# Kernel tuning notes

Measured on AMD Instinct MI355X. Metric: run time of the kernel, lower is better.

Reference implementation:

```python
import jax, jax.numpy as jnp
import numpy as np

# DLMLayer (breadth=2) forward, soft/dense path.
# Group arities: 0 (nullary [B,C0]), 1 (unary [B,n,C1]), 2 (binary [B,n,n,C2]).
# Per group i: concat [Expand(inputs[i-1]), inputs[i], Reduce(inputs[i+1])],
# then Permutation(i) (concat over i! axis permutations), then logic MLP
# (Linear -> sigmoid) over the channel dim. exclude_self masks the diagonal
# in the binary->unary reduction (max filled with 0, min filled with 1,
# valid for probabilistic truth values in [0,1]).

def setup_inputs() -> dict:
    key = jax.random.key(0)
    ks = jax.random.split(key, 9)
    B, n, C = 16, 128, 64
    x0 = jax.random.uniform(ks[0], (B, 8), dtype=jnp.float32)
    x1 = jax.random.uniform(ks[1], (B, n, C), dtype=jnp.float32)
    x2 = jax.random.uniform(ks[2], (B, n, n, C), dtype=jnp.float32)
    # current_dim per group: i=0: 8 + 2*64 = 136 ; i=1: 8 + 64 + 2*64 = 200 (1!=1)
    # i=2: (64 + 64) * 2! = 256
    W0 = jax.random.normal(ks[3], (136, C), dtype=jnp.float32) * 0.1
    W1 = jax.random.normal(ks[4], (200, C), dtype=jnp.float32) * 0.1
    W2 = jax.random.normal(ks[5], (256, C), dtype=jnp.float32) * 0.1
    b0 = jnp.zeros((C,), jnp.float32)
    b1 = jnp.zeros((C,), jnp.float32)
    b2 = jnp.zeros((C,), jnp.float32)
    return {"x0": x0, "x1": x1, "x2": x2, "W0": W0, "b0": b0,
            "W1": W1, "b1": b1, "W2": W2, "b2": b2}


def reference(x0, x1, x2, W0, b0, W1, b1, W2, b2):
    B, n, C = x1.shape
    # ---- group 0 (nullary): input x0 + reduce(x1) over the object axis ----
    r1 = jnp.concatenate([x1.max(axis=1), x1.min(axis=1)], axis=-1)  # [B, 2C]
    f0 = jnp.concatenate([x0, r1], axis=-1)                          # [B, 136]
    out0 = jax.nn.sigmoid(f0 @ W0 + b0)                              # [B, C]
    # ---- group 1 (unary): expand x0, input x1, reduce x2 (exclude self) ----
    e0 = jnp.broadcast_to(x0[:, None, :], (B, n, x0.shape[-1]))      # [B, n, 8]
    diag = jnp.eye(n, dtype=bool)[None, :, :, None]                  # [1, n, n, 1]
    rmax = jnp.where(diag, 0.0, x2).max(axis=2)                      # [B, n, C]
    rmin = jnp.where(diag, 1.0, x2).min(axis=2)                      # [B, n, C]
    f1 = jnp.concatenate([e0, x1, rmax, rmin], axis=-1)              # [B, n, 200]
    out1 = jax.nn.sigmoid(f1 @ W1 + b1)                              # [B, n, C]
    # ---- group 2 (binary): expand x1, input x2, permute axes (1,2) ----
    e1 = jnp.broadcast_to(x1[:, :, None, :], (B, n, n, C))           # [B, n, n, C]
    g = jnp.concatenate([e1, x2], axis=-1)                           # [B, n, n, 2C]
    f2 = jnp.concatenate([g, jnp.swapaxes(g, 1, 2)], axis=-1)        # [B, n, n, 4C]
    out2 = jax.nn.sigmoid(f2 @ W2 + b2)                              # [B, n, n, C]
    return (out0, out1, out2)
```

## Files before the change

kernel.cpp:

```cpp
#include <hip/hip_runtime.h>
#include <hip/hip_bf16.h>
#include <cstdint>


#define NDIM 128
#define CDIM 64

typedef float f32x4 __attribute__((ext_vector_type(4)));
typedef short s16x8 __attribute__((ext_vector_type(8)));

__device__ __forceinline__ unsigned short f2bf(float f) {
    union { float f; unsigned int u; } v; v.f = f;
    unsigned int u = v.u;
    return (unsigned short)((u + 0x7FFFu + ((u >> 16) & 1u)) >> 16);
}
__device__ __forceinline__ float sigmoidf_(float x) {
    return 1.0f / (1.0f + __expf(-x));
}

__global__ __launch_bounds__(256) void k_prep(const float* __restrict__ x0,
        const float* __restrict__ x1, const float* __restrict__ W0,
        const float* __restrict__ b0, const float* __restrict__ W2,
        const float* __restrict__ b2, float* __restrict__ PA,
        float* __restrict__ PB, unsigned short* __restrict__ WT,
        float* __restrict__ out0) {
    int bb = blockIdx.x;
    int t = threadIdx.x;
    if (bb < 512) {
        int u = t >> 6, c = t & 63;
        int blk = bb * 4 + u;
        __shared__ float xv[4][64];
        xv[u][c] = x1[blk * 64 + c];
        float accA = b2[c];
        float accB = 0.f;
#pragma unroll 8
        for (int k = 0; k < 64; ++k) {
            float xk = xv[u][k];
            accA += xk * W2[k * 64 + c];
            accB += xk * W2[(128 + k) * 64 + c];
        }
        PA[blk * 64 + c] = accA;
        PB[blk * 64 + c] = accB;
    } else if (bb < 544) {
        int idx = (bb - 512) * 256 + t;
        int n = idx >> 7, k = idx & 127;
        int row = (k < 64) ? (64 + k) : (128 + k);
        WT[idx] = f2bf(W2[row * 64 + n]);
    } else {
        int b = bb - 544;
        int lane = t & 63, w = t >> 6;
        int q = lane & 15;
        int jq = lane >> 4;
        __shared__ float pw[4][64], pn[4][64], f0[136], spart[4][64];
        f32x4 mx = {-1e30f, -1e30f, -1e30f, -1e30f};
        f32x4 mn = {1e30f, 1e30f, 1e30f, 1e30f};
#pragma unroll
        for (int p = 0; p < 8; ++p) {
            int j = (w * 4 + jq) + 16 * p;
            float4 v = *reinterpret_cast<const float4*>(
                x1 + ((size_t)(b * 128 + j)) * 64 + q * 4);
            mx.x = fmaxf(mx.x, v.x); mx.y = fmaxf(mx.y, v.y);
            mx.z = fmaxf(mx.z, v.z); mx.w = fmaxf(mx.w, v.w);
            mn.x = fminf(mn.x, v.x); mn.y = fminf(mn.y, v.y);
            mn.z = fminf(mn.z, v.z); mn.w = fminf(mn.w, v.w);
        }
#pragma unroll
        for (int d = 16; d <= 32; d <<= 1) {
            mx.x = fmaxf(mx.x, __shfl_xor(mx.x, d)); mx.y = fmaxf(mx.y, __shfl_xor(mx.y, d));
            mx.z = fmaxf(mx.z, __shfl_xor(mx.z, d)); mx.w = fmaxf(mx.w, __shfl_xor(mx.w, d));
            mn.x = fminf(mn.x, __shfl_xor(mn.x, d)); mn.y = fminf(mn.y, __shfl_xor(mn.y, d));
            mn.z = fminf(mn.z, __shfl_xor(mn.z, d)); mn.w = fminf(mn.w, __shfl_xor(mn.w, d));
        }
        if (lane < 16) {
            *reinterpret_cast<f32x4*>(&pw[w][lane * 4]) = mx;
            *reinterpret_cast<f32x4*>(&pn[w][lane * 4]) = mn;
        }
        __syncthreads();
        if (t < 64) {
            int c = t;
            float M = fmaxf(fmaxf(pw[0][c], pw[1][c]), fmaxf(pw[2][c], pw[3][c]));
            float m = fminf(fminf(pn[0][c], pn[1][c]), fminf(pn[2][c], pn[3][c]));
            f0[8 + c] = M; f0[72 + c] = m;
            if (c < 8) f0[c] = x0[b * 8 + c];
        }
        __syncthreads();
        {
            int g = t >> 6, c = t & 63;
            float acc = 0.f;
#pragma unroll
            for (int k = g * 34; k < g * 34 + 34; ++k) acc += f0[k] * W0[k * 64 + c];
            spart[g][c] = acc;
        }
        __syncthreads();
        if (t < 64) {
            int c = t;
            out0[b * 64 + c] = sigmoidf_(
                spart[0][c] + spart[1][c] + spart[2][c] + spart[3][c] + b0[c]);
        }
    }
}

__global__ __launch_bounds__(128) void k_main(const float* __restrict__ x2,
        const unsigned short* __restrict__ WT,
        const float* __restrict__ PA, const float* __restrict__ PB,
        float* __restrict__ pmax_ws, float* __restrict__ pmin_ws,
        float* __restrict__ out2) {
    int bid = blockIdx.x;
    int blk = bid >> 1, half = bid & 1;
    int b = blk >> 7, i = blk & 127;
    int j0 = half << 6;
    int t = threadIdx.x;
    int lane = t & 63, w = t >> 6;
    int jq = lane >> 4;
    int cc = (lane & 15) * 4;

    __shared__ __align__(16) unsigned short Ald[64 * 128];

    const float* xaSrc = x2 + (size_t)blk * (NDIM * CDIM);

    float4 va[8];
#pragma unroll
    for (int p = 0; p < 8; ++p) {
        int jl = 32 * w + p * 4 + jq;
        va[p] = *reinterpret_cast<const float4*>(xaSrc + (j0 + jl) * 64 + cc);
    }
    f32x4 mx = {0.f, 0.f, 0.f, 0.f}, mn = {1.f, 1.f, 1.f, 1.f};
#pragma unroll
    for (int p = 0; p < 8; ++p) {
        int jl = 32 * w + p * 4 + jq;
        bool ok = (j0 + jl != i);
        mx.x = fmaxf(mx.x, ok ? va[p].x : 0.0f); mx.y = fmaxf(mx.y, ok ? va[p].y : 0.0f);
        mx.z = fmaxf(mx.z, ok ? va[p].z : 0.0f); mx.w = fmaxf(mx.w, ok ? va[p].w : 0.0f);
        mn.x = fminf(mn.x, ok ? va[p].x : 1.0f); mn.y = fminf(mn.y, ok ? va[p].y : 1.0f);
        mn.z = fminf(mn.z, ok ? va[p].z : 1.0f); mn.w = fminf(mn.w, ok ? va[p].w : 1.0f);
        ushort4 u;
        u.x = f2bf(va[p].x); u.y = f2bf(va[p].y); u.z = f2bf(va[p].z); u.w = f2bf(va[p].w);
        *reinterpret_cast<ushort4*>(&Ald[jl * 128 + (cc ^ ((jl & 7) << 3))]) = u;
    }
#pragma unroll
    for (int d = 16; d <= 32; d <<= 1) {
        mx.x = fmaxf(mx.x, __shfl_xor(mx.x, d)); mx.y = fmaxf(mx.y, __shfl_xor(mx.y, d));
        mx.z = fmaxf(mx.z, __shfl_xor(mx.z, d)); mx.w = fmaxf(mx.w, __shfl_xor(mx.w, d));
        mn.x = fminf(mn.x, __shfl_xor(mn.x, d)); mn.y = fminf(mn.y, __shfl_xor(mn.y, d));
        mn.z = fminf(mn.z, __shfl_xor(mn.z, d)); mn.w = fminf(mn.w, __shfl_xor(mn.w, d));
    }
    if (lane < 16) {
        int slot = blk * 4 + half * 2 + w;
        *reinterpret_cast<f32x4*>(&pmax_ws[slot * 64 + cc]) = mx;
        *reinterpret_cast<f32x4*>(&pmin_ws[slot * 64 + cc]) = mn;
    }

#pragma unroll
    for (int p = 0; p < 8; ++p) {
        int jl = 32 * w + p * 4 + jq;
        float4 v = *reinterpret_cast<const float4*>(
            x2 + ((size_t)((b * 128 + j0 + jl) * 128 + i)) * 64 + cc);
        ushort4 u;
        u.x = f2bf(v.x); u.y = f2bf(v.y); u.z = f2bf(v.z); u.w = f2bf(v.w);
        *reinterpret_cast<ushort4*>(&Ald[jl * 128 + ((64 + cc) ^ ((jl & 7) << 3))]) = u;
    }

    s16x8 bfrag[4][4];
#pragma unroll
    for (int ks = 0; ks < 4; ++ks)
#pragma unroll
        for (int nt = 0; nt < 4; ++nt) {
            int n = nt * 16 + (lane & 15);
            int k0 = ks * 32 + jq * 8;
            bfrag[ks][nt] = *reinterpret_cast<const s16x8*>(WT + n * 128 + k0);
        }

    f32x4 acc[2][4];
#pragma unroll
    for (int m = 0; m < 2; ++m)
#pragma unroll
        for (int nt = 0; nt < 4; ++nt) acc[m][nt] = (f32x4){0.f, 0.f, 0.f, 0.f};

    asm volatile("s_waitcnt lgkmcnt(0)" ::: "memory");
    __builtin_amdgcn_sched_barrier(0);

#pragma unroll
    for (int ks = 0; ks < 4; ++ks) {
#pragma unroll
        for (int m = 0; m < 2; ++m) {
            int rowl = 32 * w + m * 16 + (lane & 15);
            int u8 = (ks * 4 + jq) * 8;
            s16x8 afrag = *reinterpret_cast<const s16x8*>(
                &Ald[rowl * 128 + (u8 ^ ((rowl & 7) << 3))]);
#pragma unroll
            for (int nt = 0; nt < 4; ++nt)
                acc[m][nt] = __builtin_amdgcn_mfma_f32_16x16x32_bf16(
                    afrag, bfrag[ks][nt], acc[m][nt], 0, 0, 0);
        }
    }

    const float* PAi = PA + blk * 64;
    const float* PBb = PB + b * 128 * 64;
    float* outBase = out2 + (size_t)blk * (NDIM * CDIM);
#pragma unroll
    for (int m = 0; m < 2; ++m) {
        int jt = j0 + 32 * w + m * 16 + jq * 4;
#pragma unroll
        for (int nt = 0; nt < 4; ++nt) {
            int cp = nt * 16 + (lane & 15);
            float pav = PAi[cp];
#pragma unroll
            for (int r = 0; r < 4; ++r) {
                int j = jt + r;
                outBase[j * 64 + cp] = sigmoidf_(acc[m][nt][r] + pav + PBb[j * 64 + cp]);
            }
        }
    }
}

__global__ __launch_bounds__(256) void k_out1_tail(const float* __restrict__ x0,
        const float* __restrict__ x1, const float* __restrict__ W1,
        const float* __restrict__ b1, const float* __restrict__ pmax_ws,
        const float* __restrict__ pmin_ws, float* __restrict__ out1) {
    int blk = blockIdx.x;
    int t = threadIdx.x;
    int c = t & 63, g = t >> 6;
    __shared__ float sf[200], spart[4][64];
    if (t < 64) {
        float M = 0.f, m = 1.f;
#pragma unroll
        for (int s = 0; s < 4; ++s) {
            M = fmaxf(M, pmax_ws[(blk * 4 + s) * 64 + c]);
            m = fminf(m, pmin_ws[(blk * 4 + s) * 64 + c]);
        }
        sf[72 + c] = M; sf[136 + c] = m;
        sf[8 + c] = x1[blk * 64 + c];
        if (c < 8) sf[c] = x0[(blk >> 7) * 8 + c];
    }
    __syncthreads();
    {
        float a = 0.f;
#pragma unroll 10
        for (int k = g * 50; k < g * 50 + 50; ++k) a += sf[k] * W1[k * 64 + c];
        spart[g][c] = a;
    }
    __syncthreads();
    if (t < 64) {
        out1[blk * 64 + c] = sigmoidf_(
            spart[0][c] + spart[1][c] + spart[2][c] + spart[3][c] + b1[c]);
    }
}

extern "C" void kernel_launch(void* const* d_in, const int* in_sizes, int n_in,
                              void* d_out, int out_size, void* d_ws, size_t ws_size,
                              hipStream_t stream) {
    const float* x0 = (const float*)d_in[0];
    const float* x1 = (const float*)d_in[1];
    const float* x2 = (const float*)d_in[2];
    const float* W0 = (const float*)d_in[3];
    const float* b0 = (const float*)d_in[4];
    const float* W1 = (const float*)d_in[5];
    const float* b1 = (const float*)d_in[6];
    const float* W2 = (const float*)d_in[7];
    const float* b2 = (const float*)d_in[8];

    float* out0 = (float*)d_out;
    float* out1 = out0 + 16 * 64;
    float* out2 = out1 + 16 * 128 * 64;

    float* PA = (float*)d_ws;
    float* PB = PA + 16 * 128 * 64;
    unsigned short* WT = (unsigned short*)(PB + 16 * 128 * 64);
    float* pmax_ws = (float*)(WT + 64 * 128);
    float* pmin_ws = pmax_ws + 2048 * 4 * 64;

    k_prep<<<560, 256, 0, stream>>>(x0, x1, W0, b0, W2, b2, PA, PB, WT, out0);
    k_main<<<4096, 128, 0, stream>>>(x2, WT, PA, PB, pmax_ws, pmin_ws, out2);
    k_out1_tail<<<2048, 256, 0, stream>>>(x0, x1, W1, b1, pmax_ws, pmin_ws, out1);
}
```

Measured before the change: 52.82 us.

## Split binary-group GEMM into halves to overlap transposed loads with MFMA

The strided transposed x2 loads are now issued early into registers, and the first half of the K dimension (the direct x2 half) is computed with MFMA while those loads are in flight. After that the second half is converted and written to LDS and its MFMAs run. Bf16 conversion also switches from manual bit rounding to the packed v_cvt_pk_bf16_f32 instruction. This adds register pressure (32 more VGPRs for vb plus split B fragments), which could reduce occupancy.

Result: no change. 53.30 us (+0.9%).

```diff
diff --git a/kernel.cpp b/kernel.cpp
--- a/kernel.cpp
+++ b/kernel.cpp
@@ -16,6 +16,12 @@
 }
 __device__ __forceinline__ float sigmoidf_(float x) {
     return 1.0f / (1.0f + __expf(-x));
+}
+__device__ __forceinline__ uint2 pk4(float4 v) {
+    unsigned lo, hi;
+    asm("v_cvt_pk_bf16_f32 %0, %1, %2" : "=v"(lo) : "v"(v.x), "v"(v.y));
+    asm("v_cvt_pk_bf16_f32 %0, %1, %2" : "=v"(hi) : "v"(v.z), "v"(v.w));
+    uint2 r; r.x = lo; r.y = hi; return r;
 }
 
 __global__ __launch_bounds__(256) void k_prep(const float* __restrict__ x0,
@@ -133,10 +139,18 @@
         mx.z = fmaxf(mx.z, ok ? va[p].z : 0.0f); mx.w = fmaxf(mx.w, ok ? va[p].w : 0.0f);
         mn.x = fminf(mn.x, ok ? va[p].x : 1.0f); mn.y = fminf(mn.y, ok ? va[p].y : 1.0f);
         mn.z = fminf(mn.z, ok ? va[p].z : 1.0f); mn.w = fminf(mn.w, ok ? va[p].w : 1.0f);
-        ushort4 u;
-        u.x = f2bf(va[p].x); u.y = f2bf(va[p].y); u.z = f2bf(va[p].z); u.w = f2bf(va[p].w);
-        *reinterpret_cast<ushort4*>(&Ald[jl * 128 + (cc ^ ((jl & 7) << 3))]) = u;
-    }
+        uint2 u = pk4(va[p]);
+        *reinterpret_cast<uint2*>(&Ald[jl * 128 + (cc ^ ((jl & 7) << 3))]) = u;
+    }
+
+    float4 vb[8];
+#pragma unroll
+    for (int p = 0; p < 8; ++p) {
+        int jl = 32 * w + p * 4 + jq;
+        vb[p] = *reinterpret_cast<const float4*>(
+            x2 + ((size_t)((b * 128 + j0 + jl) * 128 + i)) * 64 + cc);
+    }
+
 #pragma unroll
     for (int d = 16; d <= 32; d <<= 1) {
         mx.x = fmaxf(mx.x, __shfl_xor(mx.x, d)); mx.y = fmaxf(mx.y, __shfl_xor(mx.y, d));
@@ -150,24 +164,13 @@
         *reinterpret_cast<f32x4*>(&pmin_ws[slot * 64 + cc]) = mn;
     }
 
-#pragma unroll
-    for (int p = 0; p < 8; ++p) {
-        int jl = 32 * w + p * 4 + jq;
-        float4 v = *reinterpret_cast<const float4*>(
-            x2 + ((size_t)((b * 128 + j0 + jl) * 128 + i)) * 64 + cc);
-        ushort4 u;
-        u.x = f2bf(v.x); u.y = f2bf(v.y); u.z = f2bf(v.z); u.w = f2bf(v.w);
-        *reinterpret_cast<ushort4*>(&Ald[jl * 128 + ((64 + cc) ^ ((jl & 7) << 3))]) = u;
-    }
-
-    s16x8 bfrag[4][4];
-#pragma unroll
-    for (int ks = 0; ks < 4; ++ks)
+    s16x8 bf01[2][4];
+#pragma unroll
+    for (int ks = 0; ks < 2; ++ks)
 #pragma unroll
         for (int nt = 0; nt < 4; ++nt) {
             int n = nt * 16 + (lane & 15);
-            int k0 = ks * 32 + jq * 8;
-            bfrag[ks][nt] = *reinterpret_cast<const s16x8*>(WT + n * 128 + k0);
+            bf01[ks][nt] = *reinterpret_cast<const s16x8*>(WT + n * 128 + ks * 32 + jq * 8);
         }
 
     f32x4 acc[2][4];
@@ -180,7 +183,7 @@
     __builtin_amdgcn_sched_barrier(0);
 
 #pragma unroll
-    for (int ks = 0; ks < 4; ++ks) {
+    for (int ks = 0; ks < 2; ++ks) {
 #pragma unroll
         for (int m = 0; m < 2; ++m) {
             int rowl = 32 * w + m * 16 + (lane & 15);
@@ -190,7 +193,41 @@
 #pragma unroll
             for (int nt = 0; nt < 4; ++nt)
                 acc[m][nt] = __builtin_amdgcn_mfma_f32_16x16x32_bf16(
-                    afrag, bfrag[ks][nt], acc[m][nt], 0, 0, 0);
+                    afrag, bf01[ks][nt], acc[m][nt], 0, 0, 0);
+        }
+    }
+
+#pragma unroll
+    for (int p = 0; p < 8; ++p) {
+        int jl = 32 * w + p * 4 + jq;
+        uint2 u = pk4(vb[p]);
+        *reinterpret_cast<uint2*>(&Ald[jl * 128 + ((64 + cc) ^ ((jl & 7) << 3))]) = u;
+    }
+    s16x8 bf23[2][4];
+#pragma unroll
+    for (int ks = 0; ks < 2; ++ks)
+#pragma unroll
+        for (int nt = 0; nt < 4; ++nt) {
+            int n = nt * 16 + (lane & 15);
+            bf23[ks][nt] = *reinterpret_cast<const s16x8*>(
+                WT + n * 128 + (2 + ks) * 32 + jq * 8);
+        }
+
+    asm volatile("s_waitcnt lgkmcnt(0)" ::: "memory");
+    __builtin_amdgcn_sched_barrier(0);
+
+#pragma unroll
+    for (int ks = 0; ks < 2; ++ks) {
+#pragma unroll
+        for (int m = 0; m < 2; ++m) {
+            int rowl = 32 * w + m * 16 + (lane & 15);
+            int u8 = ((2 + ks) * 4 + jq) * 8;
+            s16x8 afrag = *reinterpret_cast<const s16x8*>(
+                &Ald[rowl * 128 + (u8 ^ ((rowl & 7) << 3))]);
+#pragma unroll
+            for (int nt = 0; nt < 4; ++nt)
+                acc[m][nt] = __builtin_amdgcn_mfma_f32_16x16x32_bf16(
+                    afrag, bf23[ks][nt], acc[m][nt], 0, 0, 0);
         }
     }
 
```

## Build MFMA fragments directly from registers, drop LDS staging, swizzle block order

Applied to the files above, without the earlier changes.

The main kernel no longer stages bf16-converted x2 rows through shared memory. Each lane now loads exactly the fp32 elements it needs for the MFMA operand and packs them with v_cvt_pk_bf16_f32. The GEMM is transposed so that weights are the A operand and data rows the B operand, which lets the epilogue write out2 with vectorized float4 stores. The masked max/min reduction is reworked to use a shuffle pattern that fits the new lane layout, and block IDs are remapped to change L2 locality. This removes LDS traffic and the waitcnt barrier, but the per-lane loads are less coalesced (eight floats per lane per row) and the scalar pmax/pmin stores go through fewer lanes.

Result: slower. 67.46 us (+27.7%).

```diff
diff --git a/kernel.cpp b/kernel.cpp
--- a/kernel.cpp
+++ b/kernel.cpp
@@ -16,6 +16,18 @@
 }
 __device__ __forceinline__ float sigmoidf_(float x) {
     return 1.0f / (1.0f + __expf(-x));
+}
+__device__ __forceinline__ uint2 pk4(float4 v) {
+    unsigned lo, hi;
+    asm("v_cvt_pk_bf16_f32 %0, %1, %2" : "=v"(lo) : "v"(v.x), "v"(v.y));
+    asm("v_cvt_pk_bf16_f32 %0, %1, %2" : "=v"(hi) : "v"(v.z), "v"(v.w));
+    uint2 r; r.x = lo; r.y = hi; return r;
+}
+__device__ __forceinline__ s16x8 mkfrag(float4 a, float4 b) {
+    uint2 p = pk4(a), q = pk4(b);
+    union { unsigned u[4]; s16x8 v; } fr;
+    fr.u[0] = p.x; fr.u[1] = p.y; fr.u[2] = q.x; fr.u[3] = q.y;
+    return fr.v;
 }
 
 __global__ __launch_bounds__(256) void k_prep(const float* __restrict__ x0,
@@ -105,92 +117,101 @@
         const float* __restrict__ PA, const float* __restrict__ PB,
         float* __restrict__ pmax_ws, float* __restrict__ pmin_ws,
         float* __restrict__ out2) {
-    int bid = blockIdx.x;
+    int bid = ((blockIdx.x & 7) << 9) | (blockIdx.x >> 3);
     int blk = bid >> 1, half = bid & 1;
     int b = blk >> 7, i = blk & 127;
     int j0 = half << 6;
     int t = threadIdx.x;
     int lane = t & 63, w = t >> 6;
-    int jq = lane >> 4;
-    int cc = (lane & 15) * 4;
-
-    __shared__ __align__(16) unsigned short Ald[64 * 128];
+    int l15 = lane & 15;
+    int lh = lane >> 4;
+
+    int jv0 = j0 + 32 * w + l15;
+    int jv1 = jv0 + 16;
 
     const float* xaSrc = x2 + (size_t)blk * (NDIM * CDIM);
-
-    float4 va[8];
-#pragma unroll
-    for (int p = 0; p < 8; ++p) {
-        int jl = 32 * w + p * 4 + jq;
-        va[p] = *reinterpret_cast<const float4*>(xaSrc + (j0 + jl) * 64 + cc);
-    }
-    f32x4 mx = {0.f, 0.f, 0.f, 0.f}, mn = {1.f, 1.f, 1.f, 1.f};
-#pragma unroll
-    for (int p = 0; p < 8; ++p) {
-        int jl = 32 * w + p * 4 + jq;
-        bool ok = (j0 + jl != i);
-        mx.x = fmaxf(mx.x, ok ? va[p].x : 0.0f); mx.y = fmaxf(mx.y, ok ? va[p].y : 0.0f);
-        mx.z = fmaxf(mx.z, ok ? va[p].z : 0.0f); mx.w = fmaxf(mx.w, ok ? va[p].w : 0.0f);
-        mn.x = fminf(mn.x, ok ? va[p].x : 1.0f); mn.y = fminf(mn.y, ok ? va[p].y : 1.0f);
-        mn.z = fminf(mn.z, ok ? va[p].z : 1.0f); mn.w = fminf(mn.w, ok ? va[p].w : 1.0f);
-        ushort4 u;
-        u.x = f2bf(va[p].x); u.y = f2bf(va[p].y); u.z = f2bf(va[p].z); u.w = f2bf(va[p].w);
-        *reinterpret_cast<ushort4*>(&Ald[jl * 128 + (cc ^ ((jl & 7) << 3))]) = u;
-    }
-#pragma unroll
-    for (int d = 16; d <= 32; d <<= 1) {
-        mx.x = fmaxf(mx.x, __shfl_xor(mx.x, d)); mx.y = fmaxf(mx.y, __shfl_xor(mx.y, d));
-        mx.z = fmaxf(mx.z, __shfl_xor(mx.z, d)); mx.w = fmaxf(mx.w, __shfl_xor(mx.w, d));
-        mn.x = fminf(mn.x, __shfl_xor(mn.x, d)); mn.y = fminf(mn.y, __shfl_xor(mn.y, d));
-        mn.z = fminf(mn.z, __shfl_xor(mn.z, d)); mn.w = fminf(mn.w, __shfl_xor(mn.w, d));
-    }
-    if (lane < 16) {
+    const float* a0 = xaSrc + jv0 * 64 + lh * 8;
+    const float* a1 = xaSrc + jv1 * 64 + lh * 8;
+    float4 va[2][2][2];
+#pragma unroll
+    for (int kw = 0; kw < 2; ++kw) {
+        va[0][kw][0] = *reinterpret_cast<const float4*>(a0 + kw * 32);
+        va[0][kw][1] = *reinterpret_cast<const float4*>(a0 + kw * 32 + 4);
+        va[1][kw][0] = *reinterpret_cast<const float4*>(a1 + kw * 32);
+        va[1][kw][1] = *reinterpret_cast<const float4*>(a1 + kw * 32 + 4);
+    }
+    const float* b0p = x2 + ((size_t)((b * 128 + jv0) * 128 + i)) * 64 + lh * 8;
+    const float* b1p = x2 + ((size_t)((b * 128 + jv1) * 128 + i)) * 64 + lh * 8;
+    float4 vb[2][2][2];
+#pragma unroll
+    for (int kw = 0; kw < 2; ++kw) {
+        vb[0][kw][0] = *reinterpret_cast<const float4*>(b0p + kw * 32);
+        vb[0][kw][1] = *reinterpret_cast<const float4*>(b0p + kw * 32 + 4);
+        vb[1][kw][0] = *reinterpret_cast<const float4*>(b1p + kw * 32);
+        vb[1][kw][1] = *reinterpret_cast<const float4*>(b1p + kw * 32 + 4);
+    }
+
+    bool ex0 = (jv0 == i), ex1 = (jv1 == i);
+    float mx[2][8], mn[2][8];
+#pragma unroll
+    for (int kw = 0; kw < 2; ++kw) {
+#pragma unroll
+        for (int e = 0; e < 8; ++e) {
+            float v0 = va[0][kw][e >> 2][e & 3];
+            float v1 = va[1][kw][e >> 2][e & 3];
+            float h0 = ex0 ? 0.f : v0, h1 = ex1 ? 0.f : v1;
+            float l0 = ex0 ? 1.f : v0, l1 = ex1 ? 1.f : v1;
+            mx[kw][e] = fmaxf(h0, h1);
+            mn[kw][e] = fminf(l0, l1);
+        }
+    }
+#pragma unroll
+    for (int d = 1; d <= 8; d <<= 1) {
+#pragma unroll
+        for (int kw = 0; kw < 2; ++kw)
+#pragma unroll
+            for (int e = 0; e < 8; ++e) {
+                mx[kw][e] = fmaxf(mx[kw][e], __shfl_xor(mx[kw][e], d));
+                mn[kw][e] = fminf(mn[kw][e], __shfl_xor(mn[kw][e], d));
+            }
+    }
+    if (l15 == 0) {
         int slot = blk * 4 + half * 2 + w;
-        *reinterpret_cast<f32x4*>(&pmax_ws[slot * 64 + cc]) = mx;
-        *reinterpret_cast<f32x4*>(&pmin_ws[slot * 64 + cc]) = mn;
-    }
-
-#pragma unroll
-    for (int p = 0; p < 8; ++p) {
-        int jl = 32 * w + p * 4 + jq;
-        float4 v = *reinterpret_cast<const float4*>(
-            x2 + ((size_t)((b * 128 + j0 + jl) * 128 + i)) * 64 + cc);
-        ushort4 u;
-        u.x = f2bf(v.x); u.y = f2bf(v.y); u.z = f2bf(v.z); u.w = f2bf(v.w);
-        *reinterpret_cast<ushort4*>(&Ald[jl * 128 + ((64 + cc) ^ ((jl & 7) << 3))]) = u;
-    }
-
-    s16x8 bfrag[4][4];
-#pragma unroll
-    for (int ks = 0; ks < 4; ++ks)
-#pragma unroll
-        for (int nt = 0; nt < 4; ++nt) {
-            int n = nt * 16 + (lane & 15);
-            int k0 = ks * 32 + jq * 8;
-            bfrag[ks][nt] = *reinterpret_cast<const s16x8*>(WT + n * 128 + k0);
-        }
-
-    f32x4 acc[2][4];
-#pragma unroll
-    for (int m = 0; m < 2; ++m)
-#pragma unroll
-        for (int nt = 0; nt < 4; ++nt) acc[m][nt] = (f32x4){0.f, 0.f, 0.f, 0.f};
-
-    asm volatile("s_waitcnt lgkmcnt(0)" ::: "memory");
-    __builtin_amdgcn_sched_barrier(0);
-
-#pragma unroll
-    for (int ks = 0; ks < 4; ++ks) {
-#pragma unroll
-        for (int m = 0; m < 2; ++m) {
-            int rowl = 32 * w + m * 16 + (lane & 15);
-            int u8 = (ks * 4 + jq) * 8;
-            s16x8 afrag = *reinterpret_cast<const s16x8*>(
-                &Ald[rowl * 128 + (u8 ^ ((rowl & 7) << 3))]);
-#pragma unroll
-            for (int nt = 0; nt < 4; ++nt)
-                acc[m][nt] = __builtin_amdgcn_mfma_f32_16x16x32_bf16(
-                    afrag, bfrag[ks][nt], acc[m][nt], 0, 0, 0);
+#pragma unroll
+        for (int kw = 0; kw < 2; ++kw) {
+            float* pmx = &pmax_ws[slot * 64 + kw * 32 + lh * 8];
+            float* pmn = &pmin_ws[slot * 64 + kw * 32 + lh * 8];
+#pragma unroll
+            for (int e = 0; e < 8; ++e) { pmx[e] = mx[kw][e]; pmn[e] = mn[kw][e]; }
+    }
+    }
+
+    s16x8 df[2][4];
+#pragma unroll
+    for (int jt = 0; jt < 2; ++jt) {
+#pragma unroll
+        for (int kw = 0; kw < 2; ++kw) {
+            df[jt][kw] = mkfrag(va[jt][kw][0], va[jt][kw][1]);
+            df[jt][2 + kw] = mkfrag(vb[jt][kw][0], vb[jt][kw][1]);
+        }
+    }
+
+    f32x4 acc[4][2];
+#pragma unroll
+    for (int mt = 0; mt < 4; ++mt)
+#pragma unroll
+        for (int jt = 0; jt < 2; ++jt) acc[mt][jt] = (f32x4){0.f, 0.f, 0.f, 0.f};
+
+    const unsigned short* wbase = WT + (size_t)l15 * 128 + lh * 8;
+#pragma unroll
+    for (int kwin = 0; kwin < 4; ++kwin) {
+#pragma unroll
+        for (int mt = 0; mt < 4; ++mt) {
+            s16x8 wf = *reinterpret_cast<const s16x8*>(wbase + mt * 16 * 128 + kwin * 32);
+#pragma unroll
+            for (int jt = 0; jt < 2; ++jt)
+                acc[mt][jt] = __builtin_amdgcn_mfma_f32_16x16x32_bf16(
+                    wf, df[jt][kwin], acc[mt][jt], 0, 0, 0);
         }
     }
 
@@ -198,17 +219,19 @@
     const float* PBb = PB + b * 128 * 64;
     float* outBase = out2 + (size_t)blk * (NDIM * CDIM);
 #pragma unroll
-    for (int m = 0; m < 2; ++m) {
-        int jt = j0 + 32 * w + m * 16 + jq * 4;
-#pragma unroll
-        for (int nt = 0; nt < 4; ++nt) {
-            int cp = nt * 16 + (lane & 15);
-            float pav = PAi[cp];
-#pragma unroll
-            for (int r = 0; r < 4; ++r) {
-                int j = jt + r;
-                outBase[j * 64 + cp] = sigmoidf_(acc[m][nt][r] + pav + PBb[j * 64 + cp]);
-            }
+    for (int jt = 0; jt < 2; ++jt) {
+        int jv = (jt == 0) ? jv0 : jv1;
+        const float* pbRow = PBb + jv * 64 + lh * 4;
+        float* outRow = outBase + jv * 64 + lh * 4;
+#pragma unroll
+        for (int mt = 0; mt < 4; ++mt) {
+            f32x4 pa4 = *reinterpret_cast<const f32x4*>(PAi + mt * 16 + lh * 4);
+            f32x4 pb4 = *reinterpret_cast<const f32x4*>(pbRow + mt * 16);
+            f32x4 o;
+#pragma unroll
+            for (int r = 0; r < 4; ++r)
+                o[r] = sigmoidf_(acc[mt][jt][r] + pa4[r] + pb4[r]);
+            *reinterpret_cast<f32x4*>(outRow + mt * 16) = o;
         }
     }
 }
```
